# Performance work log

Measured on AMD Instinct MI355X. Metric: run time of the kernel, lower is better.

The kernel has to match this reference:

```python
import jax, jax.numpy as jnp
import numpy as np


def setup_inputs() -> dict:
    key = jax.random.key(0)
    ks = jax.random.split(key, 5)
    bsz, input_size, hidden_size, level_hidden = 8192, 1024, 1024, 64
    d_in = input_size + hidden_size
    return {
        "input": jax.random.normal(ks[0], (bsz, input_size), dtype=jnp.float32),
        "h_prev": jax.random.normal(ks[1], (bsz, hidden_size), dtype=jnp.float32),
        "c_prev": jax.random.normal(ks[2], (bsz, hidden_size), dtype=jnp.float32),
        "W_lstm": jax.random.normal(ks[3], (4 * hidden_size, d_in), dtype=jnp.float32) * (1.0 / np.sqrt(d_in)),
        "W_level": jax.random.normal(ks[4], (2 * level_hidden, d_in), dtype=jnp.float32) * (1.0 / np.sqrt(d_in)),
    }


def reference(input, h_prev, c_prev, W_lstm, W_level):
    hidden_size = h_prev.shape[1]
    level_hidden = W_level.shape[0] // 2
    n_repeat = hidden_size // level_hidden

    combined = jnp.concatenate([input, h_prev], axis=-1)  # (B, in+hid)
    lstm_out = combined @ W_lstm.T                        # (B, 4*hid)
    cc_i, cc_f, cc_o, cc_g = jnp.split(lstm_out, 4, axis=1)
    level_out = combined @ W_level.T                      # (B, 2*lvl)
    cc_i_h, cc_f_h = jnp.split(level_out, 2, axis=1)

    i = jax.nn.sigmoid(cc_i)
    f = jax.nn.sigmoid(cc_f)
    o = jax.nn.sigmoid(cc_o)
    g = jnp.tanh(cc_g)

    p_f = jax.nn.softmax(cc_f_h, axis=-1)
    p_i = jax.nn.softmax(cc_i_h, axis=-1)
    f_h = jnp.cumsum(p_f, axis=-1)                         # forward cumsum
    i_h = jnp.flip(jnp.cumsum(jnp.flip(p_i, -1), axis=-1), -1)  # reverse cumsum

    # expand each level gate value across its chunk of the hidden dim
    i_h = jnp.repeat(i_h, n_repeat, axis=1)                # (B, hid)
    f_h = jnp.repeat(f_h, n_repeat, axis=1)

    w = i_h * f_h
    c = w * (f * c_prev + i * g) + (f_h - w) * c_prev + (i_h - w) * g
    h = o * jnp.tanh(c)
    return (h, c)
```

## Files before the change

### kernel.cpp

```cpp
#include <hip/hip_runtime.h>


typedef unsigned short u16;
typedef __attribute__((ext_vector_type(8))) short bf16x8;
typedef __attribute__((ext_vector_type(8))) short s8v;
typedef __attribute__((ext_vector_type(4))) float f32x4;
typedef __attribute__((ext_vector_type(4))) float v4f;

#define GLDS(g, l) __builtin_amdgcn_global_load_lds(                      \
    (const __attribute__((address_space(1))) void*)(g),                   \
    (__attribute__((address_space(3))) void*)(l), 16, 0, 0)

__device__ __forceinline__ u16 f2bf(float x) {
  unsigned u = __builtin_bit_cast(unsigned, x);
  u += 0x7FFFu + ((u >> 16) & 1u);
  return (u16)(u >> 16);
}
__device__ __forceinline__ float bf2f(u16 h) {
  unsigned u = ((unsigned)h) << 16;
  return __builtin_bit_cast(float, u);
}
__device__ __forceinline__ float fsig(float x) { return 1.0f / (1.0f + __expf(-x)); }
__device__ __forceinline__ float ftanhf(float x) { float e = __expf(2.0f * x); return 1.0f - 2.0f / (e + 1.0f); }

__global__ __launch_bounds__(256) void k_convert(
    const float* __restrict__ inp, const float* __restrict__ hprev,
    const float* __restrict__ wl, const float* __restrict__ wlev,
    u16* __restrict__ Ahi, u16* __restrict__ Whi, u16* __restrict__ Wlo)
{
  const int GA = (8192 * 2048) / 8;
  const int GW = (4224 * 2048) / 8;
  for (int gi = blockIdx.x * 256 + threadIdx.x; gi < GA + GW; gi += gridDim.x * 256) {
    if (gi < GA) {
      int e = gi << 3; int row = e >> 11, col = e & 2047;
      const float* src = (col < 1024) ? (inp + row * 1024 + col)
                                      : (hprev + row * 1024 + (col - 1024));
      v4f a = *(const v4f*)src, b = *(const v4f*)(src + 4);
      float vv[8] = {a.x, a.y, a.z, a.w, b.x, b.y, b.z, b.w};
      s8v hi;
#pragma unroll
      for (int j = 0; j < 8; ++j) hi[j] = (short)f2bf(vv[j]);
      *(s8v*)(Ahi + e) = hi;
    } else {
      int e = (gi - GA) << 3; int n = e >> 11, k = e & 2047;
      const float* src;
      if (n < 4096) { int j = n >> 2, g = n & 3; src = wl + (size_t)((g << 10) | j) * 2048 + k; }
      else          { src = wlev + (size_t)(n - 4096) * 2048 + k; }
      v4f a = *(const v4f*)src, b = *(const v4f*)(src + 4);
      float vv[8] = {a.x, a.y, a.z, a.w, b.x, b.y, b.z, b.w};
      s8v hi, lo;
#pragma unroll
      for (int j = 0; j < 8; ++j) {
        u16 h = f2bf(vv[j]);
        hi[j] = (short)h;
        lo[j] = (short)f2bf(vv[j] - bf2f(h));
      }
      *(s8v*)(Whi + e) = hi;
      if (n >= 4096) *(s8v*)(Wlo + (size_t)(n - 4096) * 2048 + k) = lo;
    }
  }
}

__global__ __launch_bounds__(256) void k_gemm_level(
    const u16* __restrict__ Ahi, const u16* __restrict__ Whi,
    const u16* __restrict__ Wlo, float* __restrict__ part)
{
  __shared__ __align__(16) u16 smem[3 * 8192];
  u16 *Ah = smem, *Bh = smem + 8192, *Bl = smem + 16384;
  const int tid = threadIdx.x, lane = tid & 63, wid = tid >> 6;
  const int wm = wid >> 1, wn = wid & 1;
  const int rm = blockIdx.x, s = blockIdx.y;
  const int lrow = lane >> 3, lcolE = (lane & 7) << 3;
  const int c16 = lane & 15, r16 = lane >> 4;
  f32x4 acc[4][4] = {};
  const u16* aBaseH = Ahi + (size_t)(rm << 7) * 2048;
  const u16* bBaseH = Whi + (size_t)4096 * 2048;

  for (int kt = 0; kt < 4; ++kt) {
    const int k0 = (s << 8) + (kt << 6);
#pragma unroll
    for (int q = 0; q < 4; ++q) {
      const int ca = (wid << 2) + q;
      size_t roff = (size_t)((ca << 3) + lrow) * 2048 + k0 + lcolE;
      GLDS(aBaseH + roff, Ah + (ca << 9));
      GLDS(bBaseH + roff, Bh + (ca << 9));
      GLDS(Wlo + roff,    Bl + (ca << 9));
    }
    __syncthreads();
#pragma unroll
    for (int ks = 0; ks < 2; ++ks) {
      bf16x8 ah[4];
#pragma unroll
      for (int i = 0; i < 4; ++i) {
        int off = ((wm << 6) + (i << 4) + c16) * 64 + (ks << 5) + (r16 << 3);
        ah[i] = *(const bf16x8*)(Ah + off);
      }
#pragma unroll
      for (int j = 0; j < 4; ++j) {
        int off = ((wn << 6) + (j << 4) + c16) * 64 + (ks << 5) + (r16 << 3);
        bf16x8 bh = *(const bf16x8*)(Bh + off);
        bf16x8 bl = *(const bf16x8*)(Bl + off);
#pragma unroll
        for (int i = 0; i < 4; ++i) {
          acc[i][j] = __builtin_amdgcn_mfma_f32_16x16x32_bf16(ah[i], bh, acc[i][j], 0, 0, 0);
          acc[i][j] = __builtin_amdgcn_mfma_f32_16x16x32_bf16(ah[i], bl, acc[i][j], 0, 0, 0);
        }
      }
    }
    __syncthreads();
  }
#pragma unroll
  for (int mi = 0; mi < 4; ++mi)
#pragma unroll
    for (int ni = 0; ni < 4; ++ni)
#pragma unroll
      for (int r = 0; r < 4; ++r) {
        int ml = (wm << 6) + (mi << 4) + (r16 << 2) + r;
        int nl = (wn << 6) + (ni << 4) + c16;
        part[(size_t)((s << 13) + (rm << 7) + ml) * 128 + nl] = acc[mi][ni][r];
      }
}

__global__ __launch_bounds__(256) void k_softmax(
    const float* __restrict__ part, float* __restrict__ ih, float* __restrict__ fh)
{
  const int tid = threadIdx.x, lane = tid & 63, w = tid >> 6;
  const int row = blockIdx.x * 4 + w;
  float vi = 0.f, vf = 0.f;
#pragma unroll
  for (int s = 0; s < 8; ++s) {
    vi += part[(size_t)((s << 13) + row) * 128 + lane];
    vf += part[(size_t)((s << 13) + row) * 128 + 64 + lane];
  }
  float mi = vi, mf = vf;
#pragma unroll
  for (int d = 1; d < 64; d <<= 1) {
    mi = fmaxf(mi, __shfl_xor(mi, d, 64));
    mf = fmaxf(mf, __shfl_xor(mf, d, 64));
  }
  float ei = __expf(vi - mi), ef = __expf(vf - mf);
  float si = ei, sf = ef;
#pragma unroll
  for (int d = 1; d < 64; d <<= 1) {
    si += __shfl_xor(si, d, 64);
    sf += __shfl_xor(sf, d, 64);
  }
  float pi = ei / si, pf = ef / sf;
  float ci = pi, cf = pf;
#pragma unroll
  for (int d = 1; d < 64; d <<= 1) {
    float t = __shfl_up(ci, d, 64); if (lane >= d) ci += t;
    float u = __shfl_up(cf, d, 64); if (lane >= d) cf += u;
  }
  ih[(row << 6) + lane] = 1.0f - (ci - pi);
  fh[(row << 6) + lane] = cf;
}

__global__ __launch_bounds__(512, 4) void k_gemm_main(
    const u16* __restrict__ Ab, const u16* __restrict__ Wb,
    const float* __restrict__ cprev, const float* __restrict__ ihp,
    const float* __restrict__ fhp, float* __restrict__ out)
{
  __shared__ __align__(16) u16 smem[36864];
  const int tid = threadIdx.x, lane = tid & 63, wid = tid >> 6;
  const int wm = wid >> 1, wn = wid & 1;
  const int c16 = lane & 15, r16 = lane >> 4;

  const int bx = blockIdx.x;
  const int nb = (bx & 7) * 128 + (bx >> 3);
  const int rm = nb >> 5, cm = nb & 31;

  const int sr = tid >> 2;
  const int slq = tid & 3;
  const int xk = (slq ^ ((sr >> 1) & 3)) << 3;
  const u16* pa = Ab + (size_t)(rm * 256 + sr) * 2048 + xk;
  const u16* pb = Wb + (size_t)(cm * 128 + sr) * 2048 + xk;
  char* const ldsW = (char*)smem + (wid << 10);

  const int xsl = (r16 ^ ((c16 >> 1) & 3)) << 3;
  const int base_a = (wm * 64 + c16) * 32 + xsl;
  const int base_b = 8192 + (wn * 64 + c16) * 32 + xsl;

  f32x4 acc[4][4] = {};

#define STAGE3(slice, slot) do {                                       \
    const u16* sa_ = pa + (slice) * 32;                                \
    const u16* sb_ = pb + (slice) * 32;                                \
    char* d_ = ldsW + (slot) * 24576;                                  \
    GLDS(sa_, d_); GLDS(sa_ + 262144, d_ + 8192);                      \
    GLDS(sb_, d_ + 16384);                                             \
  } while (0)

#define SLICE(s, slot, dostage) do {                                   \
    bf16x8 aX[4], bS[4];                                               \
    _Pragma("unroll")                                                  \
    for (int i = 0; i < 4; ++i)                                        \
      aX[i] = *(const bf16x8*)(smem + (slot) * 12288 + base_a + i * 512); \
    _Pragma("unroll")                                                  \
    for (int j = 0; j < 4; ++j)                                        \
      bS[j] = *(const bf16x8*)(smem + (slot) * 12288 + base_b + j * 512); \
    if (dostage) STAGE3(((s) + 2) & 63, ((s) + 2) % 3);                \
    asm volatile("s_waitcnt vmcnt(3)" ::: "memory");                   \
    __builtin_amdgcn_s_barrier();                                      \
    asm volatile("s_waitcnt lgkmcnt(0)" ::: "memory");                 \
    _Pragma("unroll")                                                  \
    for (int i = 0; i < 4; ++i)                                        \
      _Pragma("unroll")                                                \
      for (int j = 0; j < 4; ++j)                                      \
        acc[i][j] = __builtin_amdgcn_mfma_f32_16x16x32_bf16(           \
            aX[i], bS[j], acc[i][j], 0, 0, 0);                         \
    __builtin_amdgcn_s_barrier();                                      \
  } while (0)

  STAGE3(0, 0); STAGE3(1, 1);
  asm volatile("s_waitcnt vmcnt(3)" ::: "memory");
  __builtin_amdgcn_s_barrier();

  for (int u = 0; u < 21; ++u) {
    const int s0 = u * 3;
    SLICE(s0 + 0, 0, 1);
    SLICE(s0 + 1, 1, 1);
    SLICE(s0 + 2, 2, 1);
  }
  SLICE(63, 0, 0);
#undef SLICE
#undef STAGE3

  asm volatile("s_waitcnt vmcnt(0)" ::: "memory");
  __builtin_amdgcn_s_barrier();

  float* epi = (float*)smem;
#define EPIPASS(p) do {                                                \
    if ((wm >> 1) == (p)) {                                            \
      _Pragma("unroll")                                                \
      for (int i = 0; i < 4; ++i)                                      \
        _Pragma("unroll")                                              \
        for (int j = 0; j < 4; ++j)                                    \
          _Pragma("unroll")                                            \
          for (int r = 0; r < 4; ++r) {                                \
            float v = acc[i][j][r];                                    \
            v = ((c16 & 3) == 3) ? ftanhf(v) : fsig(v);                \
            epi[((wm & 1) * 64 + i * 16 + r16 * 4 + r) * 128 +         \
                wn * 64 + j * 16 + c16] = v;                           \
          }                                                            \
    }                                                                  \
    __syncthreads();                                                   \
    _Pragma("unroll")                                                  \
    for (int e = 0; e < 2; ++e) {                                      \
      int idx = (e << 9) + tid;                                        \
      int mrow = idx >> 3, q = idx & 7;                                \
      const float* g4 = epi + mrow * 128 + q * 16;                     \
      int rowg = rm * 256 + (p) * 128 + mrow;                          \
      int jgb = cm * 32 + q * 4;                                       \
      int lv = jgb >> 4;                                               \
      float vih = ihp[(rowg << 6) + lv], vfh = fhp[(rowg << 6) + lv];  \
      float wq = vih * vfh;                                            \
      v4f cp4 = *(const v4f*)(cprev + rowg * 1024 + jgb);              \
      float cpv[4] = {cp4.x, cp4.y, cp4.z, cp4.w};                     \
      v4f hv, cv;                                                      \
      _Pragma("unroll")                                                \
      for (int t = 0; t < 4; ++t) {                                    \
        v4f g = *(const v4f*)(g4 + t * 4);                             \
        float iv = g.x, fv = g.y, ov = g.z, gv = g.w;                  \
        float cpx = cpv[t];                                            \
        float c = wq * (fv * cpx + iv * gv) + (vfh - wq) * cpx + (vih - wq) * gv; \
        float h = ov * ftanhf(c);                                      \
        hv[t] = h; cv[t] = c;                                          \
      }                                                                \
      *(v4f*)(out + rowg * 1024 + jgb) = hv;                           \
      *(v4f*)(out + 8388608 + rowg * 1024 + jgb) = cv;                 \
    }                                                                  \
    __syncthreads();                                                   \
  } while (0)
  EPIPASS(0); EPIPASS(1);
#undef EPIPASS
}

extern "C" void kernel_launch(void* const* d_in, const int* in_sizes, int n_in,
                              void* d_out, int out_size, void* d_ws, size_t ws_size,
                              hipStream_t stream) {
  (void)in_sizes; (void)n_in; (void)out_size; (void)ws_size;
  const float* inp   = (const float*)d_in[0];
  const float* hprev = (const float*)d_in[1];
  const float* cprev = (const float*)d_in[2];
  const float* wl    = (const float*)d_in[3];
  const float* wlev  = (const float*)d_in[4];
  float* out = (float*)d_out;
  char* ws = (char*)d_ws;

  u16* Ahi  = (u16*)(ws);
  u16* Whi  = (u16*)(ws + 67108864);
  u16* Wlo  = (u16*)(ws + 84410368);
  float* part = (float*)(ws + 84934656);
  float* ih   = (float*)(ws + 118489088);
  float* fh   = (float*)(ws + 120586240);

  k_convert<<<dim3(2048), dim3(256), 0, stream>>>(inp, hprev, wl, wlev, Ahi, Whi, Wlo);
  k_gemm_level<<<dim3(64, 8), dim3(256), 0, stream>>>(Ahi, Whi, Wlo, part);
  k_softmax<<<dim3(2048), dim3(256), 0, stream>>>(part, ih, fh);
  k_gemm_main<<<dim3(1024), dim3(512), 0, stream>>>(Ahi, Whi, cprev, ih, fh, out);
}
```

Measured before the change: 209.8 us.

## Fuse level GEMM with softmax/cumsum, drop split-K partials, double-buffer loads

Replaces the split-K level GEMM plus separate softmax kernel with one kernel per 32-row tile that runs the full K=2048 reduction, double-buffering swizzled LDS tiles loaded via global_load_lds. Softmax and cumsum then run directly from LDS in the epilogue. This removes the 32 MB partial-sum buffer round trip and one kernel launch. The cost is fewer, longer-running blocks (256) with less parallelism per block, and the B tiles are reloaded by every row block.

```diff
diff --git a/kernel.cpp b/kernel.cpp
--- a/kernel.cpp
+++ b/kernel.cpp
@@ -61,99 +61,122 @@
   }
 }
 
-__global__ __launch_bounds__(256) void k_gemm_level(
+__global__ __launch_bounds__(256) void k_level_fused(
     const u16* __restrict__ Ahi, const u16* __restrict__ Whi,
-    const u16* __restrict__ Wlo, float* __restrict__ part)
+    const u16* __restrict__ Wlo, float* __restrict__ ih, float* __restrict__ fh)
 {
-  __shared__ __align__(16) u16 smem[3 * 8192];
-  u16 *Ah = smem, *Bh = smem + 8192, *Bl = smem + 16384;
+  __shared__ __align__(16) u16 smem[2 * 18432];
   const int tid = threadIdx.x, lane = tid & 63, wid = tid >> 6;
-  const int wm = wid >> 1, wn = wid & 1;
-  const int rm = blockIdx.x, s = blockIdx.y;
-  const int lrow = lane >> 3, lcolE = (lane & 7) << 3;
   const int c16 = lane & 15, r16 = lane >> 4;
-  f32x4 acc[4][4] = {};
-  const u16* aBaseH = Ahi + (size_t)(rm << 7) * 2048;
-  const u16* bBaseH = Whi + (size_t)4096 * 2048;
-
-  for (int kt = 0; kt < 4; ++kt) {
-    const int k0 = (s << 8) + (kt << 6);
-#pragma unroll
-    for (int q = 0; q < 4; ++q) {
-      const int ca = (wid << 2) + q;
-      size_t roff = (size_t)((ca << 3) + lrow) * 2048 + k0 + lcolE;
-      GLDS(aBaseH + roff, Ah + (ca << 9));
-      GLDS(bBaseH + roff, Bh + (ca << 9));
-      GLDS(Wlo + roff,    Bl + (ca << 9));
+  const int r0 = blockIdx.x << 5;
+
+  const int row_t = tid >> 3;
+  const int xk8 = ((tid & 7) ^ (row_t & 7)) << 3;
+  const u16* pa_s  = Ahi + (size_t)(r0 + row_t) * 2048 + xk8;
+  const u16* pbh_s = Whi + (size_t)(4096 + row_t) * 2048 + xk8;
+  const u16* pbl_s = Wlo + (size_t)row_t * 2048 + xk8;
+  char* const ldsW = (char*)smem + (wid << 10);
+
+  const int sl0 = ((r16 ^ (c16 & 7)) << 3);
+  const int sl1 = (((4 | r16) ^ (c16 & 7)) << 3);
+
+  f32x4 acc[2][2] = {};
+
+#define LSTAGE(kt, buf) do {                                           \
+    char* d_ = ldsW + (buf) * 36864;                                   \
+    const int ko_ = (kt) * 64;                                         \
+    GLDS(pa_s + ko_, d_);                                              \
+    GLDS(pbh_s + ko_,          d_ + 4096);                             \
+    GLDS(pbh_s + ko_ + 65536,  d_ + 8192);                             \
+    GLDS(pbh_s + ko_ + 131072, d_ + 12288);                            \
+    GLDS(pbh_s + ko_ + 196608, d_ + 16384);                            \
+    GLDS(pbl_s + ko_,          d_ + 20480);                            \
+    GLDS(pbl_s + ko_ + 65536,  d_ + 24576);                            \
+    GLDS(pbl_s + ko_ + 131072, d_ + 28672);                            \
+    GLDS(pbl_s + ko_ + 196608, d_ + 32768);                            \
+  } while (0)
+
+#define LCOMP(buf) do {                                                \
+    const u16* bp_ = smem + (buf) * 18432;                             \
+    _Pragma("unroll")                                                  \
+    for (int ks = 0; ks < 2; ++ks) {                                   \
+      const int sx_ = ks ? sl1 : sl0;                                  \
+      bf16x8 ah[2];                                                    \
+      _Pragma("unroll")                                                \
+      for (int mi = 0; mi < 2; ++mi)                                   \
+        ah[mi] = *(const bf16x8*)(bp_ + (mi * 16 + c16) * 64 + sx_);   \
+      _Pragma("unroll")                                                \
+      for (int j = 0; j < 2; ++j) {                                    \
+        int br_ = (wid * 32 + j * 16 + c16) * 64 + sx_;                \
+        bf16x8 bh = *(const bf16x8*)(bp_ + 2048 + br_);                \
+        bf16x8 bl = *(const bf16x8*)(bp_ + 10240 + br_);               \
+        _Pragma("unroll")                                              \
+        for (int mi = 0; mi < 2; ++mi) {                               \
+          acc[mi][j] = __builtin_amdgcn_mfma_f32_16x16x32_bf16(ah[mi], bh, acc[mi][j], 0, 0, 0); \
+          acc[mi][j] = __builtin_amdgcn_mfma_f32_16x16x32_bf16(ah[mi], bl, acc[mi][j], 0, 0, 0); \
+        }                                                              \
+      }                                                                \
+    }                                                                  \
+  } while (0)
+
+#define LTILE(t, buf, dostage) do {                                    \
+    if (dostage) LSTAGE((t) + 1, (buf) ^ 1);                           \
+    if (dostage) asm volatile("s_waitcnt vmcnt(9)" ::: "memory");      \
+    else         asm volatile("s_waitcnt vmcnt(0)" ::: "memory");      \
+    __builtin_amdgcn_s_barrier();                                      \
+    LCOMP(buf);                                                        \
+    __builtin_amdgcn_s_barrier();                                      \
+  } while (0)
+
+  LSTAGE(0, 0);
+  for (int u = 0; u < 15; ++u) {
+    LTILE(2 * u, 0, 1);
+    LTILE(2 * u + 1, 1, 1);
+  }
+  LTILE(30, 0, 1);
+  LTILE(31, 1, 0);
+#undef LTILE
+#undef LCOMP
+#undef LSTAGE
+
+  float* epi = (float*)smem;
+#pragma unroll
+  for (int mi = 0; mi < 2; ++mi)
+#pragma unroll
+    for (int j = 0; j < 2; ++j)
+#pragma unroll
+      for (int r = 0; r < 4; ++r)
+        epi[(mi * 16 + r16 * 4 + r) * 128 + wid * 32 + j * 16 + c16] = acc[mi][j][r];
+  __syncthreads();
+
+  for (int rr = 0; rr < 8; ++rr) {
+    int row = wid * 8 + rr;
+    float vi = epi[row * 128 + lane];
+    float vf = epi[row * 128 + 64 + lane];
+    float mi = vi, mf = vf;
+#pragma unroll
+    for (int d = 1; d < 64; d <<= 1) {
+      mi = fmaxf(mi, __shfl_xor(mi, d, 64));
+      mf = fmaxf(mf, __shfl_xor(mf, d, 64));
     }
-    __syncthreads();
-#pragma unroll
-    for (int ks = 0; ks < 2; ++ks) {
-      bf16x8 ah[4];
-#pragma unroll
-      for (int i = 0; i < 4; ++i) {
-        int off = ((wm << 6) + (i << 4) + c16) * 64 + (ks << 5) + (r16 << 3);
-        ah[i] = *(const bf16x8*)(Ah + off);
-      }
-#pragma unroll
-      for (int j = 0; j < 4; ++j) {
-        int off = ((wn << 6) + (j << 4) + c16) * 64 + (ks << 5) + (r16 << 3);
-        bf16x8 bh = *(const bf16x8*)(Bh + off);
-        bf16x8 bl = *(const bf16x8*)(Bl + off);
-#pragma unroll
-        for (int i = 0; i < 4; ++i) {
-          acc[i][j] = __builtin_amdgcn_mfma_f32_16x16x32_bf16(ah[i], bh, acc[i][j], 0, 0, 0);
-          acc[i][j] = __builtin_amdgcn_mfma_f32_16x16x32_bf16(ah[i], bl, acc[i][j], 0, 0, 0);
-        }
-      }
+    float ei = __expf(vi - mi), ef = __expf(vf - mf);
+    float si = ei, sf = ef;
+#pragma unroll
+    for (int d = 1; d < 64; d <<= 1) {
+      si += __shfl_xor(si, d, 64);
+      sf += __shfl_xor(sf, d, 64);
     }
-    __syncthreads();
+    float pi = ei / si, pf = ef / sf;
+    float ci = pi, cf = pf;
+#pragma unroll
+    for (int d = 1; d < 64; d <<= 1) {
+      float t = __shfl_up(ci, d, 64); if (lane >= d) ci += t;
+      float uu = __shfl_up(cf, d, 64); if (lane >= d) cf += uu;
+    }
+    int rowg = r0 + row;
+    ih[(rowg << 6) + lane] = 1.0f - (ci - pi);
+    fh[(rowg << 6) + lane] = cf;
   }
-#pragma unroll
-  for (int mi = 0; mi < 4; ++mi)
-#pragma unroll
-    for (int ni = 0; ni < 4; ++ni)
-#pragma unroll
-      for (int r = 0; r < 4; ++r) {
-        int ml = (wm << 6) + (mi << 4) + (r16 << 2) + r;
-        int nl = (wn << 6) + (ni << 4) + c16;
-        part[(size_t)((s << 13) + (rm << 7) + ml) * 128 + nl] = acc[mi][ni][r];
-      }
-}
-
-__global__ __launch_bounds__(256) void k_softmax(
-    const float* __restrict__ part, float* __restrict__ ih, float* __restrict__ fh)
-{
-  const int tid = threadIdx.x, lane = tid & 63, w = tid >> 6;
-  const int row = blockIdx.x * 4 + w;
-  float vi = 0.f, vf = 0.f;
-#pragma unroll
-  for (int s = 0; s < 8; ++s) {
-    vi += part[(size_t)((s << 13) + row) * 128 + lane];
-    vf += part[(size_t)((s << 13) + row) * 128 + 64 + lane];
-  }
-  float mi = vi, mf = vf;
-#pragma unroll
-  for (int d = 1; d < 64; d <<= 1) {
-    mi = fmaxf(mi, __shfl_xor(mi, d, 64));
-    mf = fmaxf(mf, __shfl_xor(mf, d, 64));
-  }
-  float ei = __expf(vi - mi), ef = __expf(vf - mf);
-  float si = ei, sf = ef;
-#pragma unroll
-  for (int d = 1; d < 64; d <<= 1) {
-    si += __shfl_xor(si, d, 64);
-    sf += __shfl_xor(sf, d, 64);
-  }
-  float pi = ei / si, pf = ef / sf;
-  float ci = pi, cf = pf;
-#pragma unroll
-  for (int d = 1; d < 64; d <<= 1) {
-    float t = __shfl_up(ci, d, 64); if (lane >= d) ci += t;
-    float u = __shfl_up(cf, d, 64); if (lane >= d) cf += u;
-  }
-  ih[(row << 6) + lane] = 1.0f - (ci - pi);
-  fh[(row << 6) + lane] = cf;
 }
 
 __global__ __launch_bounds__(512, 4) void k_gemm_main(
@@ -291,12 +314,10 @@
   u16* Ahi  = (u16*)(ws);
   u16* Whi  = (u16*)(ws + 67108864);
   u16* Wlo  = (u16*)(ws + 84410368);
-  float* part = (float*)(ws + 84934656);
   float* ih   = (float*)(ws + 118489088);
   float* fh   = (float*)(ws + 120586240);
 
   k_convert<<<dim3(2048), dim3(256), 0, stream>>>(inp, hprev, wl, wlev, Ahi, Whi, Wlo);
-  k_gemm_level<<<dim3(64, 8), dim3(256), 0, stream>>>(Ahi, Whi, Wlo, part);
-  k_softmax<<<dim3(2048), dim3(256), 0, stream>>>(part, ih, fh);
+  k_level_fused<<<dim3(256), dim3(256), 0, stream>>>(Ahi, Whi, Wlo, ih, fh);
   k_gemm_main<<<dim3(1024), dim3(512), 0, stream>>>(Ahi, Whi, cprev, ih, fh, out);
 }
```

Measured after the change: 203.6 us, median of 2. -2.9%, faster.
